# Optimization experiments

Measured on AMD Instinct MI355X. Metric: run time of the kernel, lower is better.

## Reference

```python
import jax, jax.numpy as jnp
import numpy as np

EPS = 1e-5


def _conv(x, k, pad):
    # x: (B,C,H,W), k: (Co,Ci,kh,kw)
    return jax.lax.conv_general_dilated(
        x, k, window_strides=(1, 1), padding=pad,
        dimension_numbers=("NCHW", "OIHW", "NCHW"))


def _prop_rows(x, k, b, g, bt, m, v, a, reverse):
    # direction 'D' (reverse=False) or 'U' (reverse=True).
    # conv on a 1xW stripe with 3x3 pad1 only uses the middle kernel row.
    kmid = k[:, :, 1:2, :]  # (C,C,1,3)
    # conv(current + res) = (K*current + b) + K*res ; precompute per-row part.
    pre = _conv(x, kmid, [(0, 0), (1, 1)]) + b[None, :, None, None]  # (B,C,H,W)
    inv = g / jnp.sqrt(v + EPS)
    mn, bn_b = m[None, :, None], bt[None, :, None]
    inv3 = inv[None, :, None]

    def step(res, pre_i):  # res, pre_i: (B,C,W)
        h = pre_i + _conv(res[:, :, None, :], kmid, [(0, 0), (1, 1)])[:, :, 0, :]
        y = (h - mn) * inv3 + bn_b
        y = jnp.where(y >= 0, y, a * y)  # PReLU (single shared param)
        return y, y

    B, _, H, W = x.shape
    res0 = jnp.zeros((B, k.shape[0], W), x.dtype)
    xs = jnp.moveaxis(pre, 2, 0)  # (H,B,C,W)
    _, ys = jax.lax.scan(step, res0, xs, reverse=reverse)
    return jnp.moveaxis(ys, 0, 2)  # (B,C,H,W)


def _prop_cols(x, k, b, g, bt, m, v, a, reverse):
    # direction 'R' (reverse=False) or 'L' (reverse=True); only middle kernel col used.
    kmid = k[:, :, :, 1:2]  # (C,C,3,1)
    pre = _conv(x, kmid, [(1, 1), (0, 0)]) + b[None, :, None, None]  # (B,C,H,W)
    inv = g / jnp.sqrt(v + EPS)
    mn, bn_b = m[None, :, None], bt[None, :, None]
    inv3 = inv[None, :, None]

    def step(res, pre_i):  # res, pre_i: (B,C,H)
        h = pre_i + _conv(res[:, :, :, None], kmid, [(1, 1), (0, 0)])[:, :, :, 0]
        y = (h - mn) * inv3 + bn_b
        y = jnp.where(y >= 0, y, a * y)
        return y, y

    B, _, H, W = x.shape
    res0 = jnp.zeros((B, k.shape[0], H), x.dtype)
    xs = jnp.moveaxis(pre, 3, 0)  # (W,B,C,H)
    _, ys = jax.lax.scan(step, res0, xs, reverse=reverse)
    return jnp.moveaxis(ys, 0, 3)  # (B,C,H,W)


def setup_inputs() -> dict:
    key = jax.random.key(0)
    ks = jax.random.split(key, 16)
    B, C, H, W = 8, 128, 160, 160
    x = jax.random.normal(ks[0], (B, C, H, W), jnp.float32)
    # std ~ 1/sqrt(fan_in=C*3) keeps the recurrence stable
    kernels = jax.random.normal(ks[1], (4, C, C, 3, 3), jnp.float32) * 0.04
    biases = jax.random.normal(ks[2], (4, C), jnp.float32) * 0.05
    bn_gamma = 1.0 + 0.1 * jax.random.normal(ks[3], (4, C), jnp.float32)
    bn_beta = 0.1 * jax.random.normal(ks[4], (4, C), jnp.float32)
    bn_mean = 0.1 * jax.random.normal(ks[5], (4, C), jnp.float32)
    bn_var = 1.0 + 0.1 * jax.random.uniform(ks[6], (4, C), jnp.float32)
    prelu_a = jnp.full((4,), 0.25, jnp.float32)
    fus_w = jax.random.normal(ks[7], (C, 4 * C), jnp.float32) * 0.04
    fus_b = jax.random.normal(ks[8], (C,), jnp.float32) * 0.05
    fbn_gamma = 1.0 + 0.1 * jax.random.normal(ks[9], (C,), jnp.float32)
    fbn_beta = 0.1 * jax.random.normal(ks[10], (C,), jnp.float32)
    fbn_mean = 0.1 * jax.random.normal(ks[11], (C,), jnp.float32)
    fbn_var = 1.0 + 0.1 * jax.random.uniform(ks[12], (C,), jnp.float32)
    return dict(x=x, kernels=kernels, biases=biases, bn_gamma=bn_gamma,
                bn_beta=bn_beta, bn_mean=bn_mean, bn_var=bn_var,
                prelu_a=prelu_a, fus_w=fus_w, fus_b=fus_b,
                fbn_gamma=fbn_gamma, fbn_beta=fbn_beta, fbn_mean=fbn_mean,
                fbn_var=fbn_var)


def reference(x, kernels, biases, bn_gamma, bn_beta, bn_mean, bn_var, prelu_a,
              fus_w, fus_b, fbn_gamma, fbn_beta, fbn_mean, fbn_var):
    def p(i):
        return (kernels[i], biases[i], bn_gamma[i], bn_beta[i], bn_mean[i],
                bn_var[i], prelu_a[i])

    feat_D = _prop_rows(x, *p(0), reverse=False)
    feat_U = _prop_rows(x, *p(1), reverse=True)
    feat_R = _prop_cols(x, *p(2), reverse=False)
    feat_L = _prop_cols(x, *p(3), reverse=True)
    feat = jnp.concatenate([feat_D, feat_U, feat_R, feat_L], axis=1)  # (B,4C,H,W)
    out = jnp.einsum("oc,bchw->bohw", fus_w, feat) + fus_b[None, :, None, None]
    inv = fbn_gamma / jnp.sqrt(fbn_var + EPS)
    out = (out - fbn_mean[None, :, None, None]) * inv[None, :, None, None] \
        + fbn_beta[None, :, None, None]
    return jax.nn.relu(out)
```

## Files before the change

### kernel.cpp

```cpp
#include <hip/hip_runtime.h>
#include <stdint.h>


typedef __attribute__((ext_vector_type(8))) __bf16 bf16x8;
typedef __attribute__((ext_vector_type(4))) float f32x4;

#define DEV static __device__ __forceinline__

DEV unsigned short f2bf(float f) {
  union { float f; unsigned int u; } v; v.f = f;
  unsigned int u = v.u;
  u += 0x7fffu + ((u >> 16) & 1u);
  return (unsigned short)(u >> 16);
}
DEV float bf2f(unsigned short s) {
  union { float f; unsigned int u; } v; v.u = ((unsigned int)s) << 16;
  return v.f;
}
DEV f32x4 mfma16(bf16x8 a, bf16x8 b, f32x4 c) {
  return __builtin_amdgcn_mfma_f32_16x16x32_bf16(a, b, c, 0, 0, 0);
}
DEV void barrier_lds() {
  asm volatile("s_waitcnt lgkmcnt(0)\n\ts_barrier" ::: "memory");
}

constexpr int Hc = 160, Wc = 160, Bn = 8, Cc = 128;
constexpr int CHUNK = 32, NCH = 5;
constexpr int SPAD = 136;

constexpr long WS_XT    = 0;
constexpr long WS_WPREP = 104857600;
constexpr long WS_EPI   = 105250816;
constexpr long WS_FWT   = 105254912;
constexpr long WS_FEPI  = 105385984;
constexpr long WS_FEAT  = 105387008;
constexpr long WS_EX    = 315102208;
constexpr long WS_TOTAL = 315429888;

__global__ void prep_kernel(const float* __restrict__ kern, const float* __restrict__ bias,
                            const float* __restrict__ bg, const float* __restrict__ bb,
                            const float* __restrict__ bm, const float* __restrict__ bv,
                            const float* __restrict__ fw, const float* __restrict__ fb2,
                            const float* __restrict__ fg, const float* __restrict__ fbt,
                            const float* __restrict__ fm, const float* __restrict__ fv,
                            unsigned short* __restrict__ wprep, float2* __restrict__ epi,
                            unsigned short* __restrict__ fwT, float2* __restrict__ fepi)
{
  int idx = blockIdx.x * 256 + threadIdx.x;
  if (idx < 196608) {
    int c = idx & 127;
    int t = (idx >> 7) % 3;
    int o = (idx / 384) & 127;
    int d = idx / 49152;
    int kh = (d < 2) ? 1 : t;
    int kw = (d < 2) ? t : 1;
    wprep[idx] = f2bf(kern[(((d * 128 + o) * 128 + c) * 3 + kh) * 3 + kw]);
  }
  int i2 = idx - 196608;
  if (i2 >= 0 && i2 < 65536) fwT[i2] = f2bf(fw[i2]);
  int i3 = idx - 262144;
  if (i3 >= 0 && i3 < 512) {
    float sc = bg[i3] / sqrtf(bv[i3] + 1e-5f);
    epi[i3] = make_float2(sc, (bias[i3] - bm[i3]) * sc + bb[i3]);
  }
  int i4 = idx - 262656;
  if (i4 >= 0 && i4 < 128) {
    float sc = fg[i4] / sqrtf(fv[i4] + 1e-5f);
    fepi[i4] = make_float2(sc, (fb2[i4] - fm[i4]) * sc + fbt[i4]);
  }
}

__global__ void transpose_kernel(const float* __restrict__ x, float* __restrict__ xT)
{
  __shared__ float tile[32][33];
  int b = blockIdx.z, h = blockIdx.y;
  int c0 = (blockIdx.x / 5) * 32, w0 = (blockIdx.x % 5) * 32;
  int tx = threadIdx.x & 31, ty = threadIdx.x >> 5;
#pragma unroll
  for (int r = 0; r < 4; r++) {
    int c = c0 + ty + 8 * r;
    tile[ty + 8 * r][tx] = x[(((long)b * 128 + c) * 160 + h) * 160 + w0 + tx];
  }
  __syncthreads();
#pragma unroll
  for (int r = 0; r < 4; r++) {
    int w = w0 + ty + 8 * r;
    xT[(((long)b * 160 + h) * 160 + w) * 128 + c0 + tx] = tile[tx][ty + 8 * r];
  }
}

__global__ __launch_bounds__(256, 1) void scan_kernel(
    const float* __restrict__ xT, const unsigned short* __restrict__ wprep,
    const float2* __restrict__ epi, const float* __restrict__ prelu_a,
    unsigned short* __restrict__ featbuf, unsigned int* __restrict__ ex)
{
  __shared__ unsigned short sT[34 * SPAD];

  const int bid = blockIdx.x;
  const int q = bid >> 5;
  const int g = bid & 31;
  const int d = g >> 3, b = g & 7;
  const bool row_mode = (d < 2);
  const bool rev = (d & 1);
  const int u0 = q * CHUNK;
  const int tid = threadIdx.x;
  const int lane = tid & 63;
  const int wv = tid >> 6;
  const int ncol = lane & 15;
  const int kq = lane >> 4;

  const long si = row_mode ? (long)Wc * Cc : (long)Cc;
  const long su = row_mode ? (long)Cc : (long)Wc * Cc;
  const long fi = row_mode ? (long)Wc * 512 : (long)512;
  const long fu = row_mode ? (long)512 : (long)Wc * 512;
  const float* xb = xT + (long)b * Hc * Wc * Cc;
  unsigned short* fbp = featbuf + (long)b * Hc * Wc * 512 + d * 128;

  bf16x8 Bfrag[2][12];
  float2 ep[2];
#pragma unroll
  for (int j = 0; j < 2; j++) {
    const int o = (wv * 2 + j) * 16 + ncol;
    const unsigned short* wp = wprep + ((long)(d * 128 + o)) * 384;
#pragma unroll
    for (int kt = 0; kt < 12; kt++)
      Bfrag[j][kt] = *(const bf16x8*)(wp + kt * 32 + kq * 8);
    ep[j] = epi[d * 128 + o];
  }
  const float aslope = prelu_a[d];

  unsigned int* ex_self = ex + (long)bid * 512;
  const unsigned int* ex_leftp  = ex + (long)(bid - 32) * 512 + 256;
  const unsigned int* ex_rightp = ex + (long)(bid + 32) * 512;

  const int i0 = rev ? (Hc - 1) : 0;
  for (int e = tid; e < 34 * 64; e += 256) {
    const int u = e >> 6, cp = e & 63;
    const int uu = u0 + u - 1;
    unsigned int sv = 0;
    if (uu >= 0 && uu < 160) {
      const float2 xv2 = *(const float2*)(xb + (long)i0 * si + (long)uu * su + cp * 2);
      sv = (unsigned int)f2bf(xv2.x) | ((unsigned int)f2bf(xv2.y) << 16);
    }
    *(unsigned int*)&sT[u * SPAD + cp * 2] = sv;
  }
  barrier_lds();

#pragma unroll 1
  for (int t = 0; t < 160; t++) {
    const int i = rev ? (159 - t) : t;
    const int inext = rev ? (i - 1) : (i + 1);
    const bool last = (t == 159);
    const int par = t & 1;

    float2 xv[8];
    float xh = 0.f;
    if (!last) {
#pragma unroll
      for (int rr = 0; rr < 8; rr++) {
        const int e = tid + rr * 256;
        const int u = e >> 6, cp = e & 63;
        xv[rr] = *(const float2*)(xb + (long)inext * si + (long)(u0 + u) * su + cp * 2);
      }
      const int o = tid & 127;
      const int ug = (tid < 128) ? (u0 - 1) : (u0 + CHUNK);
      if (ug >= 0 && ug < 160) xh = xb[(long)inext * si + (long)ug * su + o];
    }

    f32x4 acc[2][2];
#pragma unroll
    for (int mt = 0; mt < 2; mt++)
#pragma unroll
      for (int j = 0; j < 2; j++)
        acc[mt][j] = (f32x4){0.f, 0.f, 0.f, 0.f};
#pragma unroll
    for (int kt = 0; kt < 12; kt++) {
      const int tt = kt >> 2;
      const int c0 = ((kt & 3) << 5) + (kq << 3);
      const bf16x8 A0 = *(const bf16x8*)&sT[(ncol + tt) * SPAD + c0];
      const bf16x8 A1 = *(const bf16x8*)&sT[(16 + ncol + tt) * SPAD + c0];
      acc[0][0] = mfma16(A0, Bfrag[0][kt], acc[0][0]);
      acc[0][1] = mfma16(A0, Bfrag[1][kt], acc[0][1]);
      acc[1][0] = mfma16(A1, Bfrag[0][kt], acc[1][0]);
      acc[1][1] = mfma16(A1, Bfrag[1][kt], acc[1][1]);
    }

    unsigned short yb[2][2][4];
#pragma unroll
    for (int mt = 0; mt < 2; mt++)
#pragma unroll
      for (int j = 0; j < 2; j++)
#pragma unroll
        for (int r = 0; r < 4; r++) {
          float v = acc[mt][j][r] * ep[j].x + ep[j].y;
          v = (v >= 0.f) ? v : (aslope * v);
          yb[mt][j][r] = f2bf(v);
        }

    {
      const unsigned int tagv = ((unsigned int)(t + 1)) << 16;
      if (kq == 0) {
#pragma unroll
        for (int j = 0; j < 2; j++) {
          const int o = (wv * 2 + j) * 16 + ncol;
          __hip_atomic_store(&ex_self[par * 128 + o], tagv | (unsigned int)yb[0][j][0],
                             __ATOMIC_RELAXED, __HIP_MEMORY_SCOPE_AGENT);
        }
      }
      if (kq == 3) {
#pragma unroll
        for (int j = 0; j < 2; j++) {
          const int o = (wv * 2 + j) * 16 + ncol;
          __hip_atomic_store(&ex_self[256 + par * 128 + o], tagv | (unsigned int)yb[1][j][3],
                             __ATOMIC_RELAXED, __HIP_MEMORY_SCOPE_AGENT);
        }
      }
    }

    barrier_lds();

#pragma unroll
    for (int mt = 0; mt < 2; mt++)
#pragma unroll
      for (int j = 0; j < 2; j++)
#pragma unroll
        for (int r = 0; r < 4; r++)
          sT[(1 + mt * 16 + kq * 4 + r) * SPAD + (wv * 2 + j) * 16 + ncol] = yb[mt][j][r];

    barrier_lds();

#pragma unroll
    for (int rr = 0; rr < 8; rr++) {
      const int e = tid + rr * 256;
      const int u = e >> 6, cp = e & 63;
      const unsigned int yw = *(const unsigned int*)&sT[(1 + u) * SPAD + cp * 2];
      unsigned short* fr = fbp + (long)i * fi + (long)(u0 + u) * fu;
      ((unsigned int*)fr)[cp] = yw;
      if (!last) {
        const float y0 = bf2f((unsigned short)(yw & 0xffff));
        const float y1 = bf2f((unsigned short)(yw >> 16));
        const unsigned int sv = (unsigned int)f2bf(xv[rr].x + y0)
                              | ((unsigned int)f2bf(xv[rr].y + y1) << 16);
        *(unsigned int*)&sT[(1 + u) * SPAD + cp * 2] = sv;
      }
    }

    if (!last) {
      const int o = tid & 127;
      const bool left_side = (tid < 128);
      const int srow = left_side ? 0 : 33;
      const bool interior = left_side ? (q > 0) : (q < NCH - 1);
      float yv = 0.f;
      if (interior) {
        const unsigned int* slot = (left_side ? ex_leftp : ex_rightp) + par * 128 + o;
        unsigned int v = __hip_atomic_load(slot, __ATOMIC_RELAXED, __HIP_MEMORY_SCOPE_AGENT);
        while ((v >> 16) != (unsigned int)(t + 1)) {
          __builtin_amdgcn_s_sleep(1);
          v = __hip_atomic_load(slot, __ATOMIC_RELAXED, __HIP_MEMORY_SCOPE_AGENT);
        }
        yv = bf2f((unsigned short)(v & 0xffff));
      }
      const int ug = left_side ? (u0 - 1) : (u0 + CHUNK);
      unsigned short sv = 0;
      if (ug >= 0 && ug < 160) sv = f2bf(xh + yv);
      sT[srow * SPAD + o] = sv;
    }
    barrier_lds();
  }
}

__global__ __launch_bounds__(256, 1) void fusion_kernel(
    const unsigned short* __restrict__ featbuf, const unsigned short* __restrict__ fwT,
    const float2* __restrict__ fepi, float* __restrict__ out)
{
  __shared__ unsigned short At[32 * 520];
  const int bx = blockIdx.x;
  const int b = bx / 800, mb = bx - b * 800;
  const long m0 = (long)mb * 32;
  const int tid = threadIdx.x, lane = tid & 63, wv = tid >> 6;
  const int ncol = lane & 15, kq = lane >> 4;

  const unsigned short* fp = featbuf + ((long)b * 25600 + m0) * 512;
#pragma unroll
  for (int rr = 0; rr < 8; rr++) {
    const int e = tid + rr * 256;
    const int m = e >> 6, kp = e & 63;
    *(bf16x8*)&At[m * 520 + kp * 8] = *(const bf16x8*)(fp + (long)m * 512 + kp * 8);
  }
  bf16x8 Bf[2][16];
  float2 fe[2];
#pragma unroll
  for (int j = 0; j < 2; j++) {
    const int o = (wv * 2 + j) * 16 + ncol;
    const unsigned short* wp = fwT + (long)o * 512;
#pragma unroll
    for (int kt = 0; kt < 16; kt++)
      Bf[j][kt] = *(const bf16x8*)(wp + kt * 32 + kq * 8);
    fe[j] = fepi[o];
  }
  __syncthreads();

  f32x4 acc[2][2];
#pragma unroll
  for (int mt = 0; mt < 2; mt++)
#pragma unroll
    for (int j = 0; j < 2; j++)
      acc[mt][j] = (f32x4){0.f, 0.f, 0.f, 0.f};
#pragma unroll
  for (int kt = 0; kt < 16; kt++) {
    const bf16x8 A0 = *(const bf16x8*)&At[ncol * 520 + kt * 32 + kq * 8];
    const bf16x8 A1 = *(const bf16x8*)&At[(16 + ncol) * 520 + kt * 32 + kq * 8];
    acc[0][0] = mfma16(A0, Bf[0][kt], acc[0][0]);
    acc[0][1] = mfma16(A0, Bf[1][kt], acc[0][1]);
    acc[1][0] = mfma16(A1, Bf[0][kt], acc[1][0]);
    acc[1][1] = mfma16(A1, Bf[1][kt], acc[1][1]);
  }
#pragma unroll
  for (int mt = 0; mt < 2; mt++)
#pragma unroll
    for (int j = 0; j < 2; j++) {
      const int o = (wv * 2 + j) * 16 + ncol;
      const long hw = m0 + mt * 16 + kq * 4;
      f32x4 v;
#pragma unroll
      for (int r = 0; r < 4; r++) {
        const float z = acc[mt][j][r] * fe[j].x + fe[j].y;
        v[r] = (z > 0.f) ? z : 0.f;
      }
      *(f32x4*)(out + ((long)(b * 128 + o)) * 25600 + hw) = v;
    }
}

extern "C" void kernel_launch(void* const* d_in, const int* in_sizes, int n_in,
                              void* d_out, int out_size, void* d_ws, size_t ws_size,
                              hipStream_t stream)
{
  if (ws_size < (size_t)WS_TOTAL) return;

  const float* x        = (const float*)d_in[0];
  const float* kernels  = (const float*)d_in[1];
  const float* biases   = (const float*)d_in[2];
  const float* bn_gamma = (const float*)d_in[3];
  const float* bn_beta  = (const float*)d_in[4];
  const float* bn_mean  = (const float*)d_in[5];
  const float* bn_var   = (const float*)d_in[6];
  const float* prelu_a  = (const float*)d_in[7];
  const float* fus_w    = (const float*)d_in[8];
  const float* fus_b    = (const float*)d_in[9];
  const float* fbn_g    = (const float*)d_in[10];
  const float* fbn_b    = (const float*)d_in[11];
  const float* fbn_m    = (const float*)d_in[12];
  const float* fbn_v    = (const float*)d_in[13];

  char* ws = (char*)d_ws;
  float*          xT      = (float*)(ws + WS_XT);
  unsigned short* wprep   = (unsigned short*)(ws + WS_WPREP);
  float2*         epi     = (float2*)(ws + WS_EPI);
  unsigned short* fwT     = (unsigned short*)(ws + WS_FWT);
  float2*         fepi    = (float2*)(ws + WS_FEPI);
  unsigned short* featbuf = (unsigned short*)(ws + WS_FEAT);
  unsigned int*   ex      = (unsigned int*)(ws + WS_EX);
  float*          out     = (float*)d_out;

  prep_kernel<<<1027, 256, 0, stream>>>(kernels, biases, bn_gamma, bn_beta, bn_mean, bn_var,
                                        fus_w, fus_b, fbn_g, fbn_b, fbn_m, fbn_v,
                                        wprep, epi, fwT, fepi);
  transpose_kernel<<<dim3(20, 160, 8), 256, 0, stream>>>(x, xT);
  scan_kernel<<<160, 256, 0, stream>>>(xT, wprep, epi, prelu_a, featbuf, ex);
  fusion_kernel<<<6400, 256, 0, stream>>>(featbuf, fwT, fepi, out);
}
```

Baseline: 702.2 us.

## Double-buffer scan LDS tile and drop per-step barriers via register epilogue

The recurrent scan kernel now uses two ping-pong LDS tiles. Each step reads the current tile and writes the next step's input (x plus y) straight from the MFMA accumulator registers into the other buffer. This removes two of the three block barriers per step and the LDS round-trip used to transpose y before writing features and building the next input. The trade-off is that feature stores and next-row x loads become scattered 2-byte or 4-byte accesses following the MFMA layout rather than coalesced vector accesses. The residual is also now formed from the fp32 y instead of the bf16-rounded value, which slightly changes numerics.

```diff
diff --git a/kernel.cpp b/kernel.cpp
--- a/kernel.cpp
+++ b/kernel.cpp
@@ -94,7 +94,7 @@
     const float2* __restrict__ epi, const float* __restrict__ prelu_a,
     unsigned short* __restrict__ featbuf, unsigned int* __restrict__ ex)
 {
-  __shared__ unsigned short sT[34 * SPAD];
+  __shared__ unsigned short sbuf[2][34 * SPAD];
 
   const int bid = blockIdx.x;
   const int q = bid >> 5;
@@ -133,6 +133,16 @@
   const unsigned int* ex_leftp  = ex + (long)(bid - 32) * 512 + 256;
   const unsigned int* ex_rightp = ex + (long)(bid + 32) * 512;
 
+  const int colbase0 = (wv * 2) * 16 + ncol;
+  const int colbase1 = (wv * 2 + 1) * 16 + ncol;
+
+  const int oh = tid & 127;
+  const bool left_side = (tid < 128);
+  const int srow = left_side ? 0 : 33;
+  const bool interior = left_side ? (q > 0) : (q < NCH - 1);
+  const int ug = left_side ? (u0 - 1) : (u0 + CHUNK);
+  const bool ug_ok = (ug >= 0 && ug < 160);
+
   const int i0 = rev ? (Hc - 1) : 0;
   for (int e = tid; e < 34 * 64; e += 256) {
     const int u = e >> 6, cp = e & 63;
@@ -142,7 +152,7 @@
       const float2 xv2 = *(const float2*)(xb + (long)i0 * si + (long)uu * su + cp * 2);
       sv = (unsigned int)f2bf(xv2.x) | ((unsigned int)f2bf(xv2.y) << 16);
     }
-    *(unsigned int*)&sT[u * SPAD + cp * 2] = sv;
+    *(unsigned int*)&sbuf[0][u * SPAD + cp * 2] = sv;
   }
   barrier_lds();
 
@@ -152,19 +162,25 @@
     const int inext = rev ? (i - 1) : (i + 1);
     const bool last = (t == 159);
     const int par = t & 1;
-
-    float2 xv[8];
+    unsigned short* cur = sbuf[t & 1];
+    unsigned short* nxt = sbuf[(t & 1) ^ 1];
+
+    float xn[2][2][4];
     float xh = 0.f;
     if (!last) {
-#pragma unroll
-      for (int rr = 0; rr < 8; rr++) {
-        const int e = tid + rr * 256;
-        const int u = e >> 6, cp = e & 63;
-        xv[rr] = *(const float2*)(xb + (long)inext * si + (long)(u0 + u) * su + cp * 2);
-      }
-      const int o = tid & 127;
-      const int ug = (tid < 128) ? (u0 - 1) : (u0 + CHUNK);
-      if (ug >= 0 && ug < 160) xh = xb[(long)inext * si + (long)ug * su + o];
+      const float* xrow = xb + (long)inext * si;
+#pragma unroll
+      for (int mt = 0; mt < 2; mt++)
+#pragma unroll
+        for (int j = 0; j < 2; j++) {
+          const int col = j ? colbase1 : colbase0;
+#pragma unroll
+          for (int r = 0; r < 4; r++) {
+            const int row = mt * 16 + kq * 4 + r;
+            xn[mt][j][r] = xrow[(long)(u0 + row) * su + col];
+          }
+        }
+      if (ug_ok) xh = xrow[(long)ug * su + oh];
     }
 
     f32x4 acc[2][2];
@@ -177,14 +193,15 @@
     for (int kt = 0; kt < 12; kt++) {
       const int tt = kt >> 2;
       const int c0 = ((kt & 3) << 5) + (kq << 3);
-      const bf16x8 A0 = *(const bf16x8*)&sT[(ncol + tt) * SPAD + c0];
-      const bf16x8 A1 = *(const bf16x8*)&sT[(16 + ncol + tt) * SPAD + c0];
+      const bf16x8 A0 = *(const bf16x8*)&cur[(ncol + tt) * SPAD + c0];
+      const bf16x8 A1 = *(const bf16x8*)&cur[(16 + ncol + tt) * SPAD + c0];
       acc[0][0] = mfma16(A0, Bfrag[0][kt], acc[0][0]);
       acc[0][1] = mfma16(A0, Bfrag[1][kt], acc[0][1]);
       acc[1][0] = mfma16(A1, Bfrag[0][kt], acc[1][0]);
       acc[1][1] = mfma16(A1, Bfrag[1][kt], acc[1][1]);
     }
 
+    float yf[2][2][4];
     unsigned short yb[2][2][4];
 #pragma unroll
     for (int mt = 0; mt < 2; mt++)
@@ -194,65 +211,45 @@
         for (int r = 0; r < 4; r++) {
           float v = acc[mt][j][r] * ep[j].x + ep[j].y;
           v = (v >= 0.f) ? v : (aslope * v);
+          yf[mt][j][r] = v;
           yb[mt][j][r] = f2bf(v);
         }
 
     {
       const unsigned int tagv = ((unsigned int)(t + 1)) << 16;
       if (kq == 0) {
-#pragma unroll
-        for (int j = 0; j < 2; j++) {
-          const int o = (wv * 2 + j) * 16 + ncol;
-          __hip_atomic_store(&ex_self[par * 128 + o], tagv | (unsigned int)yb[0][j][0],
-                             __ATOMIC_RELAXED, __HIP_MEMORY_SCOPE_AGENT);
+        __hip_atomic_store(&ex_self[par * 128 + colbase0], tagv | (unsigned int)yb[0][0][0],
+                           __ATOMIC_RELAXED, __HIP_MEMORY_SCOPE_AGENT);
+        __hip_atomic_store(&ex_self[par * 128 + colbase1], tagv | (unsigned int)yb[0][1][0],
+                           __ATOMIC_RELAXED, __HIP_MEMORY_SCOPE_AGENT);
+      }
+      if (kq == 3) {
+        __hip_atomic_store(&ex_self[256 + par * 128 + colbase0], tagv | (unsigned int)yb[1][0][3],
+                           __ATOMIC_RELAXED, __HIP_MEMORY_SCOPE_AGENT);
+        __hip_atomic_store(&ex_self[256 + par * 128 + colbase1], tagv | (unsigned int)yb[1][1][3],
+                           __ATOMIC_RELAXED, __HIP_MEMORY_SCOPE_AGENT);
+      }
+    }
+
+    unsigned short* frow = fbp + (long)i * fi;
+#pragma unroll
+    for (int mt = 0; mt < 2; mt++)
+#pragma unroll
+      for (int j = 0; j < 2; j++) {
+        const int col = j ? colbase1 : colbase0;
+#pragma unroll
+        for (int r = 0; r < 4; r++) {
+          const int row = mt * 16 + kq * 4 + r;
+          frow[(long)(u0 + row) * fu + col] = yb[mt][j][r];
+          if (!last)
+            nxt[(1 + row) * SPAD + col] = f2bf(xn[mt][j][r] + yf[mt][j][r]);
         }
       }
-      if (kq == 3) {
-#pragma unroll
-        for (int j = 0; j < 2; j++) {
-          const int o = (wv * 2 + j) * 16 + ncol;
-          __hip_atomic_store(&ex_self[256 + par * 128 + o], tagv | (unsigned int)yb[1][j][3],
-                             __ATOMIC_RELAXED, __HIP_MEMORY_SCOPE_AGENT);
-        }
-      }
-    }
-
-    barrier_lds();
-
-#pragma unroll
-    for (int mt = 0; mt < 2; mt++)
-#pragma unroll
-      for (int j = 0; j < 2; j++)
-#pragma unroll
-        for (int r = 0; r < 4; r++)
-          sT[(1 + mt * 16 + kq * 4 + r) * SPAD + (wv * 2 + j) * 16 + ncol] = yb[mt][j][r];
-
-    barrier_lds();
-
-#pragma unroll
-    for (int rr = 0; rr < 8; rr++) {
-      const int e = tid + rr * 256;
-      const int u = e >> 6, cp = e & 63;
-      const unsigned int yw = *(const unsigned int*)&sT[(1 + u) * SPAD + cp * 2];
-      unsigned short* fr = fbp + (long)i * fi + (long)(u0 + u) * fu;
-      ((unsigned int*)fr)[cp] = yw;
-      if (!last) {
-        const float y0 = bf2f((unsigned short)(yw & 0xffff));
-        const float y1 = bf2f((unsigned short)(yw >> 16));
-        const unsigned int sv = (unsigned int)f2bf(xv[rr].x + y0)
-                              | ((unsigned int)f2bf(xv[rr].y + y1) << 16);
-        *(unsigned int*)&sT[(1 + u) * SPAD + cp * 2] = sv;
-      }
-    }
 
     if (!last) {
-      const int o = tid & 127;
-      const bool left_side = (tid < 128);
-      const int srow = left_side ? 0 : 33;
-      const bool interior = left_side ? (q > 0) : (q < NCH - 1);
       float yv = 0.f;
       if (interior) {
-        const unsigned int* slot = (left_side ? ex_leftp : ex_rightp) + par * 128 + o;
+        const unsigned int* slot = (left_side ? ex_leftp : ex_rightp) + par * 128 + oh;
         unsigned int v = __hip_atomic_load(slot, __ATOMIC_RELAXED, __HIP_MEMORY_SCOPE_AGENT);
         while ((v >> 16) != (unsigned int)(t + 1)) {
           __builtin_amdgcn_s_sleep(1);
@@ -260,10 +257,9 @@
         }
         yv = bf2f((unsigned short)(v & 0xffff));
       }
-      const int ug = left_side ? (u0 - 1) : (u0 + CHUNK);
       unsigned short sv = 0;
-      if (ug >= 0 && ug < 160) sv = f2bf(xh + yv);
-      sT[srow * SPAD + o] = sv;
+      if (ug_ok) sv = f2bf(xh + yv);
+      nxt[srow * SPAD + oh] = sv;
     }
     barrier_lds();
   }
```

Result: faster. 681.6 us (-2.9%).
